# Kernel optimization log

Hardware: AMD Instinct MI355X
Metric: run time of the kernel (lower is better)

Reference implementation:

```python
import jax, jax.numpy as jnp
import numpy as np


def _conv(x, w, b, stride=1, pad=0):
    # x: NCHW, w: OIHW (torch layout)
    y = jax.lax.conv_general_dilated(
        x, w, (stride, stride), [(pad, pad), (pad, pad)],
        dimension_numbers=('NCHW', 'OIHW', 'NCHW'))
    return y + b[None, :, None, None]


def _convT(x, w, b):
    # torch ConvTranspose2d(k=4, stride=2, padding=1); w: [Cin, Cout, 4, 4]
    wf = jnp.flip(w, (2, 3)).transpose(1, 0, 2, 3)  # -> OIHW
    y = jax.lax.conv_general_dilated(
        x, wf, (1, 1), [(2, 2), (2, 2)], lhs_dilation=(2, 2),
        dimension_numbers=('NCHW', 'OIHW', 'NCHW'))
    return y + b[None, :, None, None]


def _quantize(z, embed):
    # z: [B,H,W,D], embed: [D,K]  (eval-mode _Quantize: no EMA update)
    f = z.reshape(-1, z.shape[-1])
    dist = (f * f).sum(1, keepdims=True) - 2.0 * (f @ embed) + (embed * embed).sum(0, keepdims=True)
    ind = jnp.argmin(dist, axis=1)
    q = embed.T[ind].reshape(z.shape)
    diff = jnp.mean((jax.lax.stop_gradient(q) - z) ** 2)[None]
    q = z + jax.lax.stop_gradient(q - z)  # straight-through
    return q, diff, ind.reshape(z.shape[:-1])


def setup_inputs() -> dict:
    key = jax.random.key(0)
    ks = jax.random.split(key, 22)
    s = 0.02
    r = lambda k, sh, sc=s: jax.random.normal(k, sh, jnp.float32) * sc
    z = lambda sh: jnp.zeros(sh, jnp.float32)
    return {
        'x': jax.random.normal(ks[0], (16, 3, 256, 256), jnp.float32),
        # encoder_bottom: two stride-2 4x4 convs, 3->128->128 (256->64)
        'wb1': r(ks[1], (128, 3, 4, 4)), 'bb1': z(128),
        'wb2': r(ks[2], (128, 128, 4, 4)), 'bb2': z(128),
        # encoder_top: one stride-2 4x4 conv, 128->128 (64->32)
        'wt1': r(ks[3], (128, 128, 4, 4)), 'bt1': z(128),
        # quantize_conv_t: 1x1, 128->64
        'wqt': r(ks[4], (64, 128, 1, 1)), 'bqt': z(64),
        'embed_t': jax.random.normal(ks[5], (64, 512), jnp.float32),
        # decoder_top: convT 64->64 (32->64)
        'wdt': r(ks[6], (64, 64, 4, 4)), 'bdt': z(64),
        # quantize_conv_b: 1x1, 192->64
        'wqb': r(ks[7], (64, 192, 1, 1)), 'bqb': z(64),
        'embed_b': jax.random.normal(ks[8], (64, 512), jnp.float32),
        # upsample_t: convT 64->64 (32->64)
        'wup': r(ks[9], (64, 64, 4, 4)), 'bup': z(64),
        # decoder_bottom: convT 128->64 (64->128), convT 64->3 (128->256)
        'wd1': r(ks[10], (128, 64, 4, 4)), 'bd1': z(64),
        'wd2': r(ks[11], (64, 3, 4, 4)), 'bd2': z(3),
    }


def reference(x, wb1, bb1, wb2, bb2, wt1, bt1, wqt, bqt, embed_t,
              wdt, bdt, wqb, bqb, embed_b, wup, bup, wd1, bd1, wd2, bd2):
    # ----- encode -----
    enc_b = jax.nn.relu(_conv(x, wb1, bb1, stride=2, pad=1))          # [B,128,128,128]
    enc_b = jax.nn.relu(_conv(enc_b, wb2, bb2, stride=2, pad=1))      # [B,128,64,64]
    enc_t = jax.nn.relu(_conv(enc_b, wt1, bt1, stride=2, pad=1))      # [B,128,32,32]

    qt = _conv(enc_t, wqt, bqt).transpose(0, 2, 3, 1)                 # [B,32,32,64]
    quant_t, diff_t, id_t = _quantize(qt, embed_t)
    quant_t = quant_t.transpose(0, 3, 1, 2)                           # [B,64,32,32]

    dec_t = _convT(quant_t, wdt, bdt)                                 # [B,64,64,64]
    enc_cat = jnp.concatenate([dec_t, enc_b], axis=1)                 # [B,192,64,64]

    qb = _conv(enc_cat, wqb, bqb).transpose(0, 2, 3, 1)               # [B,64,64,64]
    quant_b, diff_b, id_b = _quantize(qb, embed_b)
    quant_b = quant_b.transpose(0, 3, 1, 2)                           # [B,64,64,64]

    loss_commit = diff_t + diff_b                                     # [1]

    # ----- decode -----
    up_t = _convT(quant_t, wup, bup)                                  # [B,64,64,64]
    quant = jnp.concatenate([up_t, quant_b], axis=1)                  # [B,128,64,64]
    h = jax.nn.relu(_convT(quant, wd1, bd1))                          # [B,64,128,128]
    x_hat = _convT(h, wd2, bd2)                                       # [B,3,256,256]

    return x_hat, quant_t, quant_b, loss_commit, id_t, id_b
```

## Files before the change

### kernel.cpp

```cpp
#include <hip/hip_runtime.h>

#define TPB 256

typedef __attribute__((ext_vector_type(4))) float f32x4;
typedef __attribute__((ext_vector_type(8))) short bf16x8;

__global__ void wtrans_kernel(const float* __restrict__ src, float* __restrict__ dst,
                              int CIN, int COUT, int taps, int iohw) {
    int idx = blockIdx.x * TPB + threadIdx.x;
    int tot = CIN * COUT * taps;
    if (idx >= tot) return;
    int co = idx % COUT;
    int ci = (idx / COUT) % CIN;
    int tap = idx / (COUT * CIN);
    float v = iohw ? src[(ci * COUT + co) * taps + tap]
                   : src[(co * CIN + ci) * taps + tap];
    dst[idx] = v;
}

__device__ __forceinline__ unsigned bf16_rne(float v) {
    unsigned u = __float_as_uint(v);
    return (u + 0x7FFFu + ((u >> 16) & 1u)) >> 16;
}

__global__ void wtrans_bf16_kernel(const float* __restrict__ src, short* __restrict__ dst,
                                   int CIN, int COUT, int taps, int iohw, int PL) {
    int idx = blockIdx.x * TPB + threadIdx.x;
    int tot = CIN * COUT * taps;
    if (idx >= tot) return;
    int ci = idx % CIN;
    int co = (idx / CIN) % COUT;
    int tap = idx / (CIN * COUT);
    float v = iohw ? src[(ci * COUT + co) * taps + tap]
                   : src[(co * CIN + ci) * taps + tap];
    unsigned h = bf16_rne(v);
    float rem = v - __uint_as_float(h << 16);
    dst[idx] = (short)h;
    dst[idx + PL] = (short)bf16_rne(rem);
}

__global__ void wtrans_wd2_kernel(const float* __restrict__ src, short* __restrict__ dst) {
    int idx = blockIdx.x * TPB + threadIdx.x;
    if (idx >= 16384) return;
    int ci  = idx & 63;
    int co  = (idx >> 6) & 15;
    int tap = (idx >> 10) & 3;
    int cls = idx >> 12;
    int py = cls >> 1, px = cls & 1;
    int jj = tap >> 1, ii = tap & 1;
    int ky = (1 - py) + 2 * jj;
    int kx = (1 - px) + 2 * ii;
    float v = (co < 3) ? src[(ci * 3 + co) * 16 + ky * 4 + kx] : 0.f;
    dst[idx] = (short)bf16_rne(v);
}

__global__ void etrans_kernel(const float* __restrict__ et, const float* __restrict__ eb,
                              short* __restrict__ ETt, short* __restrict__ ETb) {
    int idx = blockIdx.x * TPB + threadIdx.x;
    if (idx >= 65536) return;
    const float* src = (idx < 32768) ? et : eb;
    short* dst = (idx < 32768) ? ETt : ETb;
    int i = idx & 32767;
    int k = i & 63;
    int n = i >> 6;
    float v = src[k * 512 + n];
    unsigned h = bf16_rne(v);
    float rem = v - __uint_as_float(h << 16);
    dst[i] = (short)h;
    dst[i + 32768] = (short)bf16_rne(rem);
}

__device__ __forceinline__ void cvt_split2(float a, float b, unsigned& hw, unsigned& lw) {
    unsigned ha = bf16_rne(a), hb = bf16_rne(b);
    float ra = a - __uint_as_float(ha << 16);
    float rb = b - __uint_as_float(hb << 16);
    hw = ha | (hb << 16);
    lw = bf16_rne(ra) | (bf16_rne(rb) << 16);
}
__device__ __forceinline__ unsigned cvt_pk(float a, float b) {
    return bf16_rne(a) | (bf16_rne(b) << 16);
}

template<int ST>
__device__ __forceinline__ int lidx(int row, int koff) {
    int g  = (koff >> 3) & 3;
    int kc = koff & ~31;
    int gs = g ^ ((row >> 3) & 3);
    return row * ST + kc + (gs << 3);
}

template<int MODE, int CIN, int COUT, int SPLIT, int RELU,
         int IH, int IW, int OH, int OW, int R, int INBF, int OUTB, int KR, int NSP>
__global__ __launch_bounds__(256) void mfma_conv(
    const void* __restrict__ inv, const short* __restrict__ Wb,
    const float* __restrict__ bias, float* __restrict__ outp,
    short* __restrict__ outb) {
    constexpr int TAPS = (MODE == 0) ? 16 : (MODE == 1 ? 4 : 1);
    constexpr int CW = (MODE == 1) ? OW / 2 : OW;
    constexpr int CH = (MODE == 1) ? OH / 2 : OH;
    constexpr int NCOUT = COUT / NSP;
    constexpr int NRND = CIN / KR;
    constexpr int KC = KR / 32;
    constexpr int ST = KR + 8;
    constexpr int MTc = (NCOUT == 128) ? 4 : 2;
    constexpr long PLW = (long)TAPS * COUT * CIN;
    constexpr long APL_IN  = 16L * IH * IW * CIN;
    constexpr long APL_OUT = 16L * OH * OW * COUT;
    constexpr int NU4A = KR / 16;
    constexpr int TPR  = 256 / NCOUT;
    constexpr int SPT  = KR / TPR;
    constexpr int NU4B = SPT / 8;

    __shared__ short Ah[128 * ST];
    __shared__ short Al[SPLIT ? 128 * ST : 8];
    __shared__ short Bh[NCOUT * ST];
    __shared__ short Bl[SPLIT ? NCOUT * ST : 8];

    int bx = blockIdx.x;
    int co_off = 0;
    if (NSP == 2) {
        co_off = ((bx >> 3) & 1) * NCOUT;
        bx = (bx & 7) | ((bx >> 4) << 3);
    }
    int ry = 0, rx = 0;
    if (MODE == 1) { int c = bx & 3; ry = c >> 1; rx = c & 1; bx >>= 2; }
    const int y0 = (bx % (CH / R)) * R;
    const int n  = bx / (CH / R);

    const int tid = threadIdx.x;
    const int p   = tid >> 1;
    const int akb = (tid & 1) * (KR / 2);
    const int rr = p / CW, xx = p % CW;
    const int bco = tid / TPR;
    const int bk  = (tid % TPR) * SPT;
    const int lane = tid & 63, wv = tid >> 6;
    const int quad = lane >> 4, l16 = lane & 15;
    const int mbase = (NCOUT == 128) ? (wv & 1) * 64 : wv * 32;
    const int nbase = (NCOUT == 128) ? (wv >> 1) * 64 : 0;

    f32x4 acc[MTc][4];
#pragma unroll
    for (int mt = 0; mt < MTc; ++mt)
#pragma unroll
        for (int nt = 0; nt < 4; ++nt) acc[mt][nt] = f32x4{0.f, 0.f, 0.f, 0.f};

#pragma unroll 1
    for (int tap = 0; tap < TAPS; ++tap) {
        int iy, ix, wt;
        if (MODE == 0) {
            int ky = tap >> 2, kx = tap & 3;
            iy = 2 * (y0 + rr) - 1 + ky;
            ix = 2 * xx - 1 + kx;
            wt = tap;
        } else if (MODE == 1) {
            int jj = tap >> 1, ii = tap & 1;
            iy = (y0 + rr) + ry - jj;
            ix = xx + rx - ii;
            wt = ((1 - ry) + 2 * jj) * 4 + ((1 - rx) + 2 * ii);
        } else {
            iy = y0 + rr; ix = xx; wt = 0;
        }
        const bool av = (MODE == 2) ||
                        ((iy >= 0) && (iy < IH) && (ix >= 0) && (ix < IW));
        const long abase = ((long)(n * IH + iy) * IW + ix) * CIN + akb;

#pragma unroll 1
        for (int ko = 0; ko < NRND; ++ko) {
            __syncthreads();
            if constexpr (INBF) {
                const short* sb = (const short*)inv + abase + ko * KR;
#pragma unroll
                for (int u = 0; u < NU4A; ++u) {
                    uint4 h = av ? *(const uint4*)(sb + 8 * u) : make_uint4(0, 0, 0, 0);
                    *(uint4*)&Ah[lidx<ST>(p, akb + 8 * u)] = h;
                }
                if constexpr (SPLIT) {
#pragma unroll
                    for (int u = 0; u < NU4A; ++u) {
                        uint4 l = av ? *(const uint4*)(sb + APL_IN + 8 * u) : make_uint4(0, 0, 0, 0);
                        *(uint4*)&Al[lidx<ST>(p, akb + 8 * u)] = l;
                    }
                }
            } else {
                const float* sp = (const float*)inv + abase + ko * KR;
#pragma unroll
                for (int u = 0; u < NU4A; ++u) {
                    float4 f0, f1;
                    if (av) { f0 = *(const float4*)(sp + 8 * u); f1 = *(const float4*)(sp + 8 * u + 4); }
                    else { f0.x=f0.y=f0.z=f0.w=0.f; f1 = f0; }
                    unsigned h0, l0, h1, l1, h2, l2, h3, l3;
                    cvt_split2(f0.x, f0.y, h0, l0); cvt_split2(f0.z, f0.w, h1, l1);
                    cvt_split2(f1.x, f1.y, h2, l2); cvt_split2(f1.z, f1.w, h3, l3);
                    *(uint4*)&Ah[lidx<ST>(p, akb + 8 * u)] = make_uint4(h0, h1, h2, h3);
                    if constexpr (SPLIT)
                        *(uint4*)&Al[lidx<ST>(p, akb + 8 * u)] = make_uint4(l0, l1, l2, l3);
                }
            }
            {
                const short* wr = Wb + ((long)wt * COUT + co_off + bco) * CIN + ko * KR + bk;
#pragma unroll
                for (int u = 0; u < NU4B; ++u) {
                    *(uint4*)&Bh[lidx<ST>(bco, bk + 8 * u)] = *(const uint4*)(wr + 8 * u);
                    if constexpr (SPLIT)
                        *(uint4*)&Bl[lidx<ST>(bco, bk + 8 * u)] = *(const uint4*)(wr + PLW + 8 * u);
                }
            }
            __syncthreads();
#pragma unroll
            for (int kc = 0; kc < KC; ++kc) {
                bf16x8 ahf[MTc], alf[SPLIT ? MTc : 1];
#pragma unroll
                for (int mt = 0; mt < MTc; ++mt) {
                    int mrow = mbase + mt * 16 + l16;
                    ahf[mt] = *(const bf16x8*)&Ah[lidx<ST>(mrow, kc * 32 + quad * 8)];
                    if constexpr (SPLIT)
                        alf[mt] = *(const bf16x8*)&Al[lidx<ST>(mrow, kc * 32 + quad * 8)];
                }
#pragma unroll
                for (int nt = 0; nt < 4; ++nt) {
                    int nrow = nbase + nt * 16 + l16;
                    bf16x8 bhf = *(const bf16x8*)&Bh[lidx<ST>(nrow, kc * 32 + quad * 8)];
#pragma unroll
                    for (int mt = 0; mt < MTc; ++mt)
                        acc[mt][nt] = __builtin_amdgcn_mfma_f32_16x16x32_bf16(ahf[mt], bhf, acc[mt][nt], 0, 0, 0);
                    if constexpr (SPLIT) {
                        bf16x8 blf = *(const bf16x8*)&Bl[lidx<ST>(nrow, kc * 32 + quad * 8)];
#pragma unroll
                        for (int mt = 0; mt < MTc; ++mt) {
                            acc[mt][nt] = __builtin_amdgcn_mfma_f32_16x16x32_bf16(alf[mt], bhf, acc[mt][nt], 0, 0, 0);
                            acc[mt][nt] = __builtin_amdgcn_mfma_f32_16x16x32_bf16(ahf[mt], blf, acc[mt][nt], 0, 0, 0);
                        }
                    }
                }
            }
        }
    }
#pragma unroll
    for (int mt = 0; mt < MTc; ++mt)
#pragma unroll
        for (int nt = 0; nt < 4; ++nt) {
            int co = co_off + nbase + nt * 16 + l16;
            float bv = bias[co];
#pragma unroll
            for (int r = 0; r < 4; ++r) {
                int pl = mbase + mt * 16 + quad * 4 + r;
                int rr2 = pl / CW, x2 = pl % CW;
                int oy, ox;
                if (MODE == 1) { oy = 2 * (y0 + rr2) + ry; ox = 2 * x2 + rx; }
                else           { oy = y0 + rr2; ox = x2; }
                float vv = acc[mt][nt][r] + bv;
                if (RELU) vv = fmaxf(vv, 0.f);
                long oidx = ((long)(n * OH + oy) * OW + ox) * COUT + co;
                if constexpr (OUTB == 0) outp[oidx] = vv;
                if constexpr (OUTB == 3) {
                    unsigned hh = bf16_rne(vv);
                    outb[oidx] = (short)hh;
                    outb[oidx + APL_OUT] = (short)bf16_rne(vv - __uint_as_float(hh << 16));
                }
                if constexpr (OUTB == 2) outb[oidx] = (short)bf16_rne(vv);
            }
        }
}

template<int MODE, int CIN, int COUT, int BM, int RELU, int IH, int IW, int OH, int OW>
__global__ __launch_bounds__(256) void conv_gemm(
    const float* __restrict__ in, const float* __restrict__ Wt,
    const float* __restrict__ bias, float* __restrict__ out) {
    constexpr int CHUNK  = 64;
    constexpr int NCH    = CIN / CHUNK;
    constexpr int CO_PER = (COUT == 128) ? 4 : 2;
    constexpr int PX_PER = BM / 8;
    constexpr int TAPS   = (MODE == 0) ? 16 : (MODE == 1 ? 4 : 1);
    __shared__ float As[CHUNK * BM];
    __shared__ float Bs[CHUNK * COUT];
    const int tid = threadIdx.x;
    const int bx  = blockIdx.x;
    int n, oy, ox0 = 0, par = 0;
    if (MODE == 1) {
        par = bx & 1;
        oy  = (bx >> 1) % OH;
        n   = bx / (2 * OH);
    } else {
        constexpr int SPR = OW / BM;
        int s = bx % SPR;
        oy = (bx / SPR) % OH;
        n  = bx / (SPR * OH);
        ox0 = s * BM;
    }
    const int cog = tid & 31;
    const int pxg = tid >> 5;
    const int co0 = cog * CO_PER, px0 = pxg * PX_PER;
    float acc[PX_PER][CO_PER];
#pragma unroll
    for (int q = 0; q < PX_PER; ++q)
#pragma unroll
        for (int j = 0; j < CO_PER; ++j) acc[q][j] = 0.f;
    constexpr int TPX  = 256 / BM;
    constexpr int CIPT = CHUNK / TPX;
    const int spx  = tid / TPX;
    const int sci0 = (tid % TPX) * CIPT;
    const int py   = oy & 1;

#pragma unroll 1
    for (int tap = 0; tap < TAPS; ++tap) {
        int iy, twi, sx;
        if (MODE == 0) {
            int ky = tap >> 2, kx = tap & 3;
            iy  = 2 * oy - 1 + ky;
            sx  = 2 * (ox0 + spx) - 1 + kx;
            twi = tap;
        } else if (MODE == 1) {
            int jj = tap >> 1, ii = tap & 1;
            iy  = ((oy + 1) >> 1) - jj;
            sx  = spx + par - ii;
            twi = ((1 - py) + 2 * jj) * 4 + ((1 - par) + 2 * ii);
        } else {
            iy = oy; sx = ox0 + spx; twi = 0;
        }
        const bool pxv = (iy >= 0) && (iy < IH) && (sx >= 0) && (sx < IW);
        const float* srcp = in + (((long)n * IH + iy) * IW + sx) * CIN + sci0;
#pragma unroll 1
        for (int cb = 0; cb < NCH; ++cb) {
            __syncthreads();
            float4 tmp[CIPT / 4];
#pragma unroll
            for (int t4 = 0; t4 < CIPT / 4; ++t4) {
                if (pxv) tmp[t4] = *(const float4*)(srcp + cb * CHUNK + 4 * t4);
                else { tmp[t4].x = 0.f; tmp[t4].y = 0.f; tmp[t4].z = 0.f; tmp[t4].w = 0.f; }
            }
#pragma unroll
            for (int t4 = 0; t4 < CIPT / 4; ++t4) {
                As[(sci0 + 4 * t4 + 0) * BM + spx] = tmp[t4].x;
                As[(sci0 + 4 * t4 + 1) * BM + spx] = tmp[t4].y;
                As[(sci0 + 4 * t4 + 2) * BM + spx] = tmp[t4].z;
                As[(sci0 + 4 * t4 + 3) * BM + spx] = tmp[t4].w;
            }
            {
                const float4* wsrc = (const float4*)(Wt + ((long)twi * CIN + cb * CHUNK) * COUT);
#pragma unroll
                for (int t4 = 0; t4 < (CHUNK * COUT) / 1024; ++t4)
                    ((float4*)Bs)[tid + 256 * t4] = wsrc[tid + 256 * t4];
            }
            __syncthreads();
#pragma unroll 4
            for (int k = 0; k < CHUNK; ++k) {
                float a[PX_PER];
#pragma unroll
                for (int t4 = 0; t4 < PX_PER / 4; ++t4)
                    *(float4*)&a[4 * t4] = *(const float4*)&As[k * BM + px0 + 4 * t4];
                if constexpr (CO_PER == 4) {
                    float4 b = *(const float4*)&Bs[k * COUT + co0];
#pragma unroll
                    for (int q = 0; q < PX_PER; ++q) {
                        acc[q][0] = fmaf(a[q], b.x, acc[q][0]);
                        acc[q][1] = fmaf(a[q], b.y, acc[q][1]);
                        acc[q][2] = fmaf(a[q], b.z, acc[q][2]);
                        acc[q][3] = fmaf(a[q], b.w, acc[q][3]);
                    }
                } else {
                    float2 b = *(const float2*)&Bs[k * COUT + co0];
#pragma unroll
                    for (int q = 0; q < PX_PER; ++q) {
                        acc[q][0] = fmaf(a[q], b.x, acc[q][0]);
                        acc[q][1] = fmaf(a[q], b.y, acc[q][1]);
                    }
                }
            }
        }
    }
    float bv[CO_PER];
#pragma unroll
    for (int j = 0; j < CO_PER; ++j) bv[j] = bias[co0 + j];
#pragma unroll
    for (int q = 0; q < PX_PER; ++q) {
        int ox = (MODE == 1) ? (par + 2 * (px0 + q)) : (ox0 + px0 + q);
        float* op = out + (((long)n * OH + oy) * OW + ox) * COUT + co0;
        if constexpr (CO_PER == 4) {
            float4 v;
            v.x = acc[q][0] + bv[0]; v.y = acc[q][1] + bv[1];
            v.z = acc[q][2] + bv[2]; v.w = acc[q][3] + bv[3];
            if (RELU) { v.x = fmaxf(v.x, 0.f); v.y = fmaxf(v.y, 0.f);
                        v.z = fmaxf(v.z, 0.f); v.w = fmaxf(v.w, 0.f); }
            *(float4*)op = v;
        } else {
            float2 v;
            v.x = acc[q][0] + bv[0]; v.y = acc[q][1] + bv[1];
            if (RELU) { v.x = fmaxf(v.x, 0.f); v.y = fmaxf(v.y, 0.f); }
            *(float2*)op = v;
        }
    }
}

__global__ __launch_bounds__(256) void convt_final_mfma(
    const short* __restrict__ h, const short* __restrict__ Wc,
    const float* __restrict__ bias, float* __restrict__ out) {
    const int HW = 128;
    __shared__ short HB[3 * 130 * 72];
    __shared__ float Sout[6 * 260];

    const int tid = threadIdx.x;
    const int y = blockIdx.x & 127;
    const int n = blockIdx.x >> 7;
    const int lane = tid & 63, wv = tid >> 6;
    const int quad = lane >> 4, l16 = lane & 15;

    for (int u = tid; u < 780; u += TPB) {
        int row = u >> 1, half = u & 1;
        int hr = row / 130, xc = row % 130;
        int hy = y - 1 + hr, hx = xc - 1;
        bool ok = (hy >= 0 && hy < HW && hx >= 0 && hx < HW);
        const short* sp = h + ((long)(n * HW + hy) * HW + hx) * 64 + half * 32;
        uint4 a0, a1, a2, a3;
        if (ok) {
            a0 = *(const uint4*)sp;        a1 = *(const uint4*)(sp + 8);
            a2 = *(const uint4*)(sp + 16); a3 = *(const uint4*)(sp + 24);
        } else {
            a0 = make_uint4(0,0,0,0); a1 = a0; a2 = a0; a3 = a0;
        }
        short* dp = &HB[row * 72 + half * 32];
        *(uint4*)dp = a0; *(uint4*)(dp + 8) = a1;
        *(uint4*)(dp + 16) = a2; *(uint4*)(dp + 24) = a3;
    }
    __syncthreads();

#pragma unroll 1
    for (int cls = 0; cls < 4; ++cls) {
        const int py = cls >> 1, px = cls & 1;
        bf16x8 Bf[4][2];
#pragma unroll
        for (int tap = 0; tap < 4; ++tap)
#pragma unroll
            for (int cb = 0; cb < 2; ++cb)
                Bf[tap][cb] = *(const bf16x8*)&Wc[((cls * 4 + tap) * 16 + l16) * 64 + cb * 32 + quad * 8];

        f32x4 acc2[2] = { f32x4{0.f,0.f,0.f,0.f}, f32x4{0.f,0.f,0.f,0.f} };
#pragma unroll
        for (int mt = 0; mt < 2; ++mt) {
            const int xp0 = wv * 32 + mt * 16;
#pragma unroll
            for (int tap = 0; tap < 4; ++tap) {
                const int jj = tap >> 1, ii = tap & 1;
                const int hr = py - jj + 1;
                const int rbase = (hr * 130 + xp0 + l16 + px - ii + 1) * 72;
#pragma unroll
                for (int cb = 0; cb < 2; ++cb) {
                    bf16x8 Af = *(const bf16x8*)&HB[rbase + cb * 32 + quad * 8];
                    acc2[mt] = __builtin_amdgcn_mfma_f32_16x16x32_bf16(Af, Bf[tap][cb], acc2[mt], 0, 0, 0);
                }
            }
        }
        if (l16 < 3) {
#pragma unroll
            for (int mt = 0; mt < 2; ++mt)
#pragma unroll
                for (int r = 0; r < 4; ++r) {
                    int xp = wv * 32 + mt * 16 + quad * 4 + r;
                    Sout[(py * 3 + l16) * 260 + 2 * xp + px] = acc2[mt][r];
                }
        }
    }
    __syncthreads();

    for (int u = tid; u < 384; u += TPB) {
        int idx = u * 4;
        int rowi = idx >> 8;
        int xq   = idx & 255;
        int py = rowi / 3, co = rowi % 3;
        float bv = bias[co];
        float4 v = *(const float4*)&Sout[rowi * 260 + xq];
        v.x += bv; v.y += bv; v.z += bv; v.w += bv;
        *(float4*)&out[(((long)(n * 3 + co) * 256) + 2 * y + py) * 256 + xq] = v;
    }
}

__global__ __launch_bounds__(256) void conv1_kernel(
    const float* __restrict__ x, const float* __restrict__ Wt,
    const float* __restrict__ bias, short* __restrict__ outb) {
    const int IH = 256, IW = 256, OH = 128, OW = 128, BM = 64;
    const long APL0 = 16L * 128 * 128 * 128;
    int bx = blockIdx.x;
    int sx = bx & 1;
    int oy = (bx >> 1) & 127;
    int n  = bx >> 8;
    int ox0 = sx * BM;
    __shared__ float Bs[16 * 3 * 128];
    __shared__ float Ts[3 * 4 * 132];
    int tid = threadIdx.x;
    for (int i = tid; i < 6144 / 4; i += TPB)
        ((float4*)Bs)[i] = ((const float4*)Wt)[i];
    int iy0 = 2 * oy - 1;
    for (int idx = tid; idx < 3 * 4 * 130; idx += TPB) {
        int ci = idx / 520; int r = idx % 520;
        int ky = r / 130;   int xx = r % 130;
        int iy = iy0 + ky;  int ix = 2 * ox0 - 1 + xx;
        float v = 0.f;
        if (iy >= 0 && iy < IH && ix >= 0 && ix < IW)
            v = x[((n * 3 + ci) * IH + iy) * IW + ix];
        Ts[(ci * 4 + ky) * 132 + xx] = v;
    }
    __syncthreads();
    int cog = tid & 31, pxg = tid >> 5;
    int co0 = cog * 4, px0 = pxg * 8;
    float acc[8][4];
#pragma unroll
    for (int i = 0; i < 8; ++i)
#pragma unroll
        for (int j = 0; j < 4; ++j) acc[i][j] = 0.f;
#pragma unroll 1
    for (int ky = 0; ky < 4; ++ky)
#pragma unroll 1
        for (int kx = 0; kx < 4; ++kx)
#pragma unroll
            for (int ci = 0; ci < 3; ++ci) {
                float4 b = *(const float4*)&Bs[((ky * 4 + kx) * 3 + ci) * 128 + co0];
                const float* trow = &Ts[(ci * 4 + ky) * 132 + kx];
#pragma unroll
                for (int q = 0; q < 8; ++q) {
                    float a = trow[2 * (px0 + q)];
                    acc[q][0] = fmaf(a, b.x, acc[q][0]);
                    acc[q][1] = fmaf(a, b.y, acc[q][1]);
                    acc[q][2] = fmaf(a, b.z, acc[q][2]);
                    acc[q][3] = fmaf(a, b.w, acc[q][3]);
                }
            }
    float4 bb = *(const float4*)&bias[co0];
#pragma unroll
    for (int q = 0; q < 8; ++q) {
        int ox = ox0 + px0 + q;
        float v0 = fmaxf(acc[q][0] + bb.x, 0.f);
        float v1 = fmaxf(acc[q][1] + bb.y, 0.f);
        float v2 = fmaxf(acc[q][2] + bb.z, 0.f);
        float v3 = fmaxf(acc[q][3] + bb.w, 0.f);
        unsigned h0, l0, h1, l1;
        cvt_split2(v0, v1, h0, l0);
        cvt_split2(v2, v3, h1, l1);
        long pix = ((long)n * OH + oy) * OW + ox;
        *(uint2*)&outb[pix * 128 + co0]        = make_uint2(h0, h1);
        *(uint2*)&outb[APL0 + pix * 128 + co0] = make_uint2(l0, l1);
    }
}

__global__ void enorm_kernel(const float* __restrict__ et, const float* __restrict__ eb,
                             float* __restrict__ nt, float* __restrict__ nb) {
    int k = blockIdx.x * TPB + threadIdx.x;
    if (k >= 1024) return;
    const float* e = (k < 512) ? et : eb;
    float* o = (k < 512) ? nt : nb;
    int kk = k & 511;
    float s = 0.f;
#pragma unroll 8
    for (int d = 0; d < 64; ++d) { float v = e[d * 512 + kk]; s = fmaf(v, v, s); }
    o[kk] = s;
}

__global__ __launch_bounds__(256) void quantize_mfma(
    const float* __restrict__ f, const short* __restrict__ ET,
    const float* __restrict__ embed, const float* __restrict__ enorm,
    float* __restrict__ qn, short* __restrict__ qnb, float* __restrict__ qc,
    float* __restrict__ ido, float* __restrict__ dsum, int M, int HW) {
    __shared__ short Fh[64 * 72];
    __shared__ short Fl[64 * 72];
    __shared__ float S[64 * 65];
    __shared__ int   KI[64];
    __shared__ float wsum[4];

    const int tid = threadIdx.x;
    const int lane = tid & 63, wv = tid >> 6;
    const int quad = lane >> 4, l16 = lane & 15;
    const int R0 = blockIdx.x * 64;

    {
        int row = tid >> 2;
        int k0 = (tid & 3) * 16;
        const float* sp = f + (long)(R0 + row) * 64 + k0;
        unsigned hw[8], lw[8];
#pragma unroll
        for (int i = 0; i < 4; ++i) {
            float4 p = *(const float4*)(sp + 4 * i);
            cvt_split2(p.x, p.y, hw[2 * i], lw[2 * i]);
            cvt_split2(p.z, p.w, hw[2 * i + 1], lw[2 * i + 1]);
        }
        short* dh = &Fh[row * 72 + k0];
        short* dl = &Fl[row * 72 + k0];
        *(uint4*)(dh)     = make_uint4(hw[0], hw[1], hw[2], hw[3]);
        *(uint4*)(dh + 8) = make_uint4(hw[4], hw[5], hw[6], hw[7]);
        *(uint4*)(dl)     = make_uint4(lw[0], lw[1], lw[2], lw[3]);
        *(uint4*)(dl + 8) = make_uint4(lw[4], lw[5], lw[6], lw[7]);
    }
    __syncthreads();

    const int arow = (wv * 16 + l16) * 72;
    bf16x8 Ah0 = *(const bf16x8*)&Fh[arow + quad * 8];
    bf16x8 Ah1 = *(const bf16x8*)&Fh[arow + 32 + quad * 8];
    bf16x8 Al0 = *(const bf16x8*)&Fl[arow + quad * 8];
    bf16x8 Al1 = *(const bf16x8*)&Fl[arow + 32 + quad * 8];

    float bestv[4];
    int   besti[4];
#pragma unroll
    for (int r = 0; r < 4; ++r) { bestv[r] = 3.4e38f; besti[r] = 0; }

    const short* ETlo = ET + 32768;
#pragma unroll 2
    for (int j = 0; j < 32; ++j) {
        const int nb = (j * 16 + l16) * 64 + quad * 8;
        bf16x8 Bh0 = *(const bf16x8*)(ET + nb);
        bf16x8 Bh1 = *(const bf16x8*)(ET + nb + 32);
        bf16x8 Bl0 = *(const bf16x8*)(ETlo + nb);
        bf16x8 Bl1 = *(const bf16x8*)(ETlo + nb + 32);
        f32x4 acc = f32x4{0.f, 0.f, 0.f, 0.f};
        acc = __builtin_amdgcn_mfma_f32_16x16x32_bf16(Ah0, Bh0, acc, 0, 0, 0);
        acc = __builtin_amdgcn_mfma_f32_16x16x32_bf16(Ah1, Bh1, acc, 0, 0, 0);
        acc = __builtin_amdgcn_mfma_f32_16x16x32_bf16(Al0, Bh0, acc, 0, 0, 0);
        acc = __builtin_amdgcn_mfma_f32_16x16x32_bf16(Al1, Bh1, acc, 0, 0, 0);
        acc = __builtin_amdgcn_mfma_f32_16x16x32_bf16(Ah0, Bl0, acc, 0, 0, 0);
        acc = __builtin_amdgcn_mfma_f32_16x16x32_bf16(Ah1, Bl1, acc, 0, 0, 0);
        float en = enorm[j * 16 + l16];
        int   ni = j * 16 + l16;
#pragma unroll
        for (int r = 0; r < 4; ++r) {
            float s = fmaf(-2.f, acc[r], en);
            if (s < bestv[r]) { bestv[r] = s; besti[r] = ni; }
        }
    }
#pragma unroll
    for (int m = 1; m < 16; m <<= 1) {
#pragma unroll
        for (int r = 0; r < 4; ++r) {
            float ov = __shfl_xor(bestv[r], m);
            int   oi = __shfl_xor(besti[r], m);
            if (ov < bestv[r] || (ov == bestv[r] && oi < besti[r])) {
                bestv[r] = ov; besti[r] = oi;
            }
        }
    }
    if (l16 == 0) {
#pragma unroll
        for (int r = 0; r < 4; ++r) KI[wv * 16 + quad * 4 + r] = besti[r];
    }
    __syncthreads();

    float ddacc = 0.f;
#pragma unroll 1
    for (int r16 = 0; r16 < 16; ++r16) {
        int row = wv * 16 + r16;
        int k = KI[row];
        float ev = embed[lane * 512 + k];
        float fv = f[(long)(R0 + row) * 64 + lane];
        long qi = (long)(R0 + row) * 64 + lane;
        qn[qi] = ev;
        qnb[qi] = (short)bf16_rne(ev);
        S[row * 65 + lane] = ev;
        float dq = ev - fv;
        ddacc = fmaf(dq, dq, ddacc);
        if (lane == 0) ido[R0 + row] = (float)k;
    }
#pragma unroll
    for (int off = 1; off < 64; off <<= 1) ddacc += __shfl_xor(ddacc, off);
    if (lane == 0) wsum[wv] = ddacc;
    __syncthreads();
    if (tid == 0)
        atomicAdd(dsum, wsum[0] + wsum[1] + wsum[2] + wsum[3]);

    int nn = R0 / HW;
    int rem0 = R0 - nn * HW;
    int px = tid & 63;
    int cg = tid >> 6;
#pragma unroll
    for (int it = 0; it < 16; ++it) {
        int c = cg + 4 * it;
        qc[((long)nn * 64 + c) * HW + rem0 + px] = S[px * 65 + c];
    }
}

__global__ void concat_rec_kernel(const float* __restrict__ a, const short* __restrict__ bh,
                                  float* __restrict__ o, int M) {
    const long PLB = 8388608L;
    int idx = blockIdx.x * TPB + threadIdx.x;
    if (idx >= M * 48) return;
    int row = idx / 48;
    int c4  = (idx - row * 48) * 4;
    float4 v;
    if (c4 < 64) v = *(const float4*)(a + (long)row * 64 + c4);
    else {
        int cc = c4 - 64;
        uint2 h = *(const uint2*)(bh + (long)row * 128 + cc);
        uint2 l = *(const uint2*)(bh + PLB + (long)row * 128 + cc);
        v.x = __uint_as_float(h.x << 16)         + __uint_as_float(l.x << 16);
        v.y = __uint_as_float(h.x & 0xFFFF0000u) + __uint_as_float(l.x & 0xFFFF0000u);
        v.z = __uint_as_float(h.y << 16)         + __uint_as_float(l.y << 16);
        v.w = __uint_as_float(h.y & 0xFFFF0000u) + __uint_as_float(l.y & 0xFFFF0000u);
    }
    *(float4*)(o + (long)row * 192 + c4) = v;
}

__global__ void concat_qcat_kernel(const float* __restrict__ a, const short* __restrict__ qh,
                                   short* __restrict__ o, int M) {
    int idx = blockIdx.x * TPB + threadIdx.x;
    if (idx >= M * 32) return;
    int row = idx / 32;
    int c4  = (idx - row * 32) * 4;
    uint2 w;
    if (c4 < 64) {
        float4 v = *(const float4*)(a + (long)row * 64 + c4);
        w = make_uint2(cvt_pk(v.x, v.y), cvt_pk(v.z, v.w));
    } else {
        w = *(const uint2*)(qh + (long)row * 64 + (c4 - 64));
    }
    *(uint2*)(o + (long)row * 128 + c4) = w;
}

__global__ void loss_kernel(const float* __restrict__ sums, float* __restrict__ out) {
    out[0] = sums[0] * (1.f / (16384.f * 64.f)) + sums[1] * (1.f / (65536.f * 64.f));
}

extern "C" void kernel_launch(void* const* d_in, const int* in_sizes, int n_in,
                              void* d_out, int out_size, void* d_ws, size_t ws_size,
                              hipStream_t stream) {
    const float* x   = (const float*)d_in[0];
    const float* wb1 = (const float*)d_in[1];  const float* bb1 = (const float*)d_in[2];
    const float* wb2 = (const float*)d_in[3];  const float* bb2 = (const float*)d_in[4];
    const float* wt1 = (const float*)d_in[5];  const float* bt1 = (const float*)d_in[6];
    const float* wqt = (const float*)d_in[7];  const float* bqt = (const float*)d_in[8];
    const float* embed_t = (const float*)d_in[9];
    const float* wdt = (const float*)d_in[10]; const float* bdt = (const float*)d_in[11];
    const float* wqb = (const float*)d_in[12]; const float* bqb = (const float*)d_in[13];
    const float* embed_b = (const float*)d_in[14];
    const float* wup = (const float*)d_in[15]; const float* bup = (const float*)d_in[16];
    const float* wd1 = (const float*)d_in[17]; const float* bd1 = (const float*)d_in[18];
    const float* wd2 = (const float*)d_in[19]; const float* bd2 = (const float*)d_in[20];
    float* out = (float*)d_out;
    float* ws  = (float*)d_ws;

    float* O_XHAT = out;
    float* O_QT   = out + 3145728;
    float* O_QB   = out + 4194304;
    float* O_LOSS = out + 8388608;
    float* O_IDT  = out + 8388609;
    float* O_IDB  = out + 8404993;

    float* W_WB1  = ws + 0;
    short* WB_WD2 = (short*)(ws + 16384);
    short* ET_T   = (short*)(ws + 32768);
    short* ET_B   = (short*)(ws + 65536);
    short* WB_WQT = (short*)(ws + 98304);
    float* W_WDT  = ws + 540672;
    float* W_WQB  = ws + 606208;
    float* EN_T  = ws + 818176;
    float* EN_B  = ws + 818688;
    float* SUMS  = ws + 819200;
    short* T1B   = (short*)(ws + 1048576);
    const long BIG = 9437184;
    short* T0B   = (short*)(ws + BIG);
    short* T2B   = (short*)(ws + BIG);
    float* QT    = ws + BIG + 2097152;
    float* QTN   = ws + BIG + 3145728;
    short* QTNB  = (short*)(ws + BIG + 4194304);
    float* DECT  = ws + BIG + 4718592;
    float* ECAT  = ws + BIG + 8912896;
    float* QB    = ws + BIG + 21495808;
    short* QBNB  = (short*)(ws + BIG + 25690112);
    float* QND   = ws + BIG + 27787264;
    float* UPT   = ws + BIG + 4718592;
    short* QCATB = (short*)(ws + BIG + 8912896);
    short* HBUFB = (short*)(ws + BIG + 16777216);
    short* WB_BF2 = (short*)(ws + 42991616);
    short* WB_BT1 = (short*)(ws + 43253760);
    short* WB_BD1 = (short*)(ws + 43515904);
    short* WB_BUP = (short*)(ws + 43646976);

    auto wt_launch = [&](const float* src, float* dst, int cin, int cout, int taps, int iohw) {
        int tot = cin * cout * taps;
        wtrans_kernel<<<(tot + TPB - 1) / TPB, TPB, 0, stream>>>(src, dst, cin, cout, taps, iohw);
    };
    auto wtb_launch = [&](const float* src, short* dst, int cin, int cout, int taps, int iohw) {
        int tot = cin * cout * taps;
        wtrans_bf16_kernel<<<(tot + TPB - 1) / TPB, TPB, 0, stream>>>(src, dst, cin, cout, taps, iohw, tot);
    };
    wt_launch(wb1, W_WB1, 3, 128, 16, 0);
    wt_launch(wdt, W_WDT, 64, 64, 16, 1);
    wt_launch(wqb, W_WQB, 192, 64, 1, 0);
    wtrans_wd2_kernel<<<64, TPB, 0, stream>>>(wd2, WB_WD2);
    wtb_launch(wb2, WB_BF2, 128, 128, 16, 0);
    wtb_launch(wt1, WB_BT1, 128, 128, 16, 0);
    wtb_launch(wqt, WB_WQT, 128, 64, 1, 0);
    wtb_launch(wd1, WB_BD1, 128, 64, 16, 1);
    wtb_launch(wup, WB_BUP, 64, 64, 16, 1);
    enorm_kernel<<<4, TPB, 0, stream>>>(embed_t, embed_b, EN_T, EN_B);
    etrans_kernel<<<256, TPB, 0, stream>>>(embed_t, embed_b, ET_T, ET_B);
    hipError_t e0 = hipMemsetAsync((void*)SUMS, 0, 2 * sizeof(float), stream);
    (void)e0;

    conv1_kernel<<<4096, TPB, 0, stream>>>(x, W_WB1, bb1, T0B);
    mfma_conv<0, 128, 128, 1, 1, 128, 128, 64, 64, 2, 1, 3, 32, 2>
        <<<1024, TPB, 0, stream>>>(T0B, WB_BF2, bb2, nullptr, T1B);
    mfma_conv<0, 128, 128, 1, 1, 64, 64, 32, 32, 4, 1, 3, 32, 2>
        <<<256, TPB, 0, stream>>>(T1B, WB_BT1, bt1, nullptr, T2B);
    mfma_conv<2, 128, 64, 1, 0, 32, 32, 32, 32, 4, 1, 0, 64, 1>
        <<<128, TPB, 0, stream>>>(T2B, WB_WQT, bqt, QT, nullptr);
    quantize_mfma<<<256, TPB, 0, stream>>>(QT, ET_T, embed_t, EN_T, QTN, QTNB,
                                           O_QT, O_IDT, SUMS, 16384, 1024);
    conv_gemm<1, 64, 64, 32, 0, 32, 32, 64, 64><<<2048, TPB, 0, stream>>>(QTN, W_WDT, bdt, DECT);
    concat_rec_kernel<<<12288, TPB, 0, stream>>>(DECT, T1B, ECAT, 65536);
    conv_gemm<2, 192, 64, 64, 0, 64, 64, 64, 64><<<1024, TPB, 0, stream>>>(ECAT, W_WQB, bqb, QB);
    quantize_mfma<<<1024, TPB, 0, stream>>>(QB, ET_B, embed_b, EN_B, QND, QBNB,
                                            O_QB, O_IDB, SUMS + 1, 65536, 4096);
    mfma_conv<1, 64, 64, 0, 0, 32, 32, 64, 64, 4, 1, 0, 64, 1>
        <<<512, TPB, 0, stream>>>(QTNB, WB_BUP, bup, UPT, nullptr);
    concat_qcat_kernel<<<8192, TPB, 0, stream>>>(UPT, QBNB, QCATB, 65536);
    mfma_conv<1, 128, 64, 0, 1, 64, 64, 128, 128, 2, 1, 2, 64, 1>
        <<<2048, TPB, 0, stream>>>(QCATB, WB_BD1, bd1, nullptr, HBUFB);
    convt_final_mfma<<<2048, TPB, 0, stream>>>(HBUFB, WB_WD2, bd2, O_XHAT);
    loss_kernel<<<1, 1, 0, stream>>>(SUMS, O_LOSS);

    (void)in_sizes; (void)n_in; (void)out_size; (void)ws_size;
}
```

Measured before the change: 718.8 us.

## Drop LDS swizzle, skip unused fp32 quant write, widen conv2 cout tile

Removes the XOR swizzle from the shared-memory tile indexing in mfma_conv and uses plain padded row-major addressing (ST = KR+8). The bottom quantizer no longer writes its fp32 quantized copy to a scratch buffer that nothing reads, which cuts global store traffic. The second encoder conv now covers all 128 output channels per block (NSP=1, half the blocks), so each input tile is loaded once instead of twice. Without the swizzle, LDS bank conflicts may return, and the larger per-block tile lowers parallelism and occupancy.

```diff
diff --git a/kernel.cpp b/kernel.cpp
--- a/kernel.cpp
+++ b/kernel.cpp
@@ -79,14 +79,6 @@
 }
 __device__ __forceinline__ unsigned cvt_pk(float a, float b) {
     return bf16_rne(a) | (bf16_rne(b) << 16);
-}
-
-template<int ST>
-__device__ __forceinline__ int lidx(int row, int koff) {
-    int g  = (koff >> 3) & 3;
-    int kc = koff & ~31;
-    int gs = g ^ ((row >> 3) & 3);
-    return row * ST + kc + (gs << 3);
 }
 
 template<int MODE, int CIN, int COUT, int SPLIT, int RELU,
@@ -172,13 +164,13 @@
 #pragma unroll
                 for (int u = 0; u < NU4A; ++u) {
                     uint4 h = av ? *(const uint4*)(sb + 8 * u) : make_uint4(0, 0, 0, 0);
-                    *(uint4*)&Ah[lidx<ST>(p, akb + 8 * u)] = h;
+                    *(uint4*)&Ah[p * ST + akb + 8 * u] = h;
                 }
                 if constexpr (SPLIT) {
 #pragma unroll
                     for (int u = 0; u < NU4A; ++u) {
                         uint4 l = av ? *(const uint4*)(sb + APL_IN + 8 * u) : make_uint4(0, 0, 0, 0);
-                        *(uint4*)&Al[lidx<ST>(p, akb + 8 * u)] = l;
+                        *(uint4*)&Al[p * ST + akb + 8 * u] = l;
                     }
                 }
             } else {
@@ -191,18 +183,18 @@
                     unsigned h0, l0, h1, l1, h2, l2, h3, l3;
                     cvt_split2(f0.x, f0.y, h0, l0); cvt_split2(f0.z, f0.w, h1, l1);
                     cvt_split2(f1.x, f1.y, h2, l2); cvt_split2(f1.z, f1.w, h3, l3);
-                    *(uint4*)&Ah[lidx<ST>(p, akb + 8 * u)] = make_uint4(h0, h1, h2, h3);
+                    *(uint4*)&Ah[p * ST + akb + 8 * u] = make_uint4(h0, h1, h2, h3);
                     if constexpr (SPLIT)
-                        *(uint4*)&Al[lidx<ST>(p, akb + 8 * u)] = make_uint4(l0, l1, l2, l3);
+                        *(uint4*)&Al[p * ST + akb + 8 * u] = make_uint4(l0, l1, l2, l3);
                 }
             }
             {
                 const short* wr = Wb + ((long)wt * COUT + co_off + bco) * CIN + ko * KR + bk;
 #pragma unroll
                 for (int u = 0; u < NU4B; ++u) {
-                    *(uint4*)&Bh[lidx<ST>(bco, bk + 8 * u)] = *(const uint4*)(wr + 8 * u);
+                    *(uint4*)&Bh[bco * ST + bk + 8 * u] = *(const uint4*)(wr + 8 * u);
                     if constexpr (SPLIT)
-                        *(uint4*)&Bl[lidx<ST>(bco, bk + 8 * u)] = *(const uint4*)(wr + PLW + 8 * u);
+                        *(uint4*)&Bl[bco * ST + bk + 8 * u] = *(const uint4*)(wr + PLW + 8 * u);
                 }
             }
             __syncthreads();
@@ -212,19 +204,19 @@
 #pragma unroll
                 for (int mt = 0; mt < MTc; ++mt) {
                     int mrow = mbase + mt * 16 + l16;
-                    ahf[mt] = *(const bf16x8*)&Ah[lidx<ST>(mrow, kc * 32 + quad * 8)];
+                    ahf[mt] = *(const bf16x8*)&Ah[mrow * ST + kc * 32 + quad * 8];
                     if constexpr (SPLIT)
-                        alf[mt] = *(const bf16x8*)&Al[lidx<ST>(mrow, kc * 32 + quad * 8)];
+                        alf[mt] = *(const bf16x8*)&Al[mrow * ST + kc * 32 + quad * 8];
                 }
 #pragma unroll
                 for (int nt = 0; nt < 4; ++nt) {
                     int nrow = nbase + nt * 16 + l16;
-                    bf16x8 bhf = *(const bf16x8*)&Bh[lidx<ST>(nrow, kc * 32 + quad * 8)];
+                    bf16x8 bhf = *(const bf16x8*)&Bh[nrow * ST + kc * 32 + quad * 8];
 #pragma unroll
                     for (int mt = 0; mt < MTc; ++mt)
                         acc[mt][nt] = __builtin_amdgcn_mfma_f32_16x16x32_bf16(ahf[mt], bhf, acc[mt][nt], 0, 0, 0);
                     if constexpr (SPLIT) {
-                        bf16x8 blf = *(const bf16x8*)&Bl[lidx<ST>(nrow, kc * 32 + quad * 8)];
+                        bf16x8 blf = *(const bf16x8*)&Bl[nrow * ST + kc * 32 + quad * 8];
 #pragma unroll
                         for (int mt = 0; mt < MTc; ++mt) {
                             acc[mt][nt] = __builtin_amdgcn_mfma_f32_16x16x32_bf16(alf[mt], bhf, acc[mt][nt], 0, 0, 0);
@@ -648,7 +640,7 @@
         float ev = embed[lane * 512 + k];
         float fv = f[(long)(R0 + row) * 64 + lane];
         long qi = (long)(R0 + row) * 64 + lane;
-        qn[qi] = ev;
+        if (qn) qn[qi] = ev;
         qnb[qi] = (short)bf16_rne(ev);
         S[row * 65 + lane] = ev;
         float dq = ev - fv;
@@ -760,7 +752,6 @@
     float* ECAT  = ws + BIG + 8912896;
     float* QB    = ws + BIG + 21495808;
     short* QBNB  = (short*)(ws + BIG + 25690112);
-    float* QND   = ws + BIG + 27787264;
     float* UPT   = ws + BIG + 4718592;
     short* QCATB = (short*)(ws + BIG + 8912896);
     short* HBUFB = (short*)(ws + BIG + 16777216);
@@ -792,8 +783,8 @@
     (void)e0;
 
     conv1_kernel<<<4096, TPB, 0, stream>>>(x, W_WB1, bb1, T0B);
-    mfma_conv<0, 128, 128, 1, 1, 128, 128, 64, 64, 2, 1, 3, 32, 2>
-        <<<1024, TPB, 0, stream>>>(T0B, WB_BF2, bb2, nullptr, T1B);
+    mfma_conv<0, 128, 128, 1, 1, 128, 128, 64, 64, 2, 1, 3, 32, 1>
+        <<<512, TPB, 0, stream>>>(T0B, WB_BF2, bb2, nullptr, T1B);
     mfma_conv<0, 128, 128, 1, 1, 64, 64, 32, 32, 4, 1, 3, 32, 2>
         <<<256, TPB, 0, stream>>>(T1B, WB_BT1, bt1, nullptr, T2B);
     mfma_conv<2, 128, 64, 1, 0, 32, 32, 32, 32, 4, 1, 0, 64, 1>
@@ -803,7 +794,7 @@
     conv_gemm<1, 64, 64, 32, 0, 32, 32, 64, 64><<<2048, TPB, 0, stream>>>(QTN, W_WDT, bdt, DECT);
     concat_rec_kernel<<<12288, TPB, 0, stream>>>(DECT, T1B, ECAT, 65536);
     conv_gemm<2, 192, 64, 64, 0, 64, 64, 64, 64><<<1024, TPB, 0, stream>>>(ECAT, W_WQB, bqb, QB);
-    quantize_mfma<<<1024, TPB, 0, stream>>>(QB, ET_B, embed_b, EN_B, QND, QBNB,
+    quantize_mfma<<<1024, TPB, 0, stream>>>(QB, ET_B, embed_b, EN_B, nullptr, QBNB,
                                             O_QB, O_IDB, SUMS + 1, 65536, 4096);
     mfma_conv<1, 64, 64, 0, 0, 32, 32, 64, 64, 4, 1, 0, 64, 1>
         <<<512, TPB, 0, stream>>>(QTNB, WB_BUP, bup, UPT, nullptr);
```

Result: faster. 702.5 us (-2.3%).
